# Optimization experiments

Measured on AMD Instinct MI355X. Metric: run time of the kernel, lower is better.

Reference implementation:

```python
import jax, jax.numpy as jnp
import numpy as np

D_MODEL = 1024
N_HEADS = 16
HEAD = D_MODEL // N_HEADS
B, T = 4, 2048


def setup_inputs() -> dict:
    key = jax.random.key(0)
    ks = jax.random.split(key, 8)
    s = 0.02
    return {
        "x_enc": jax.random.normal(ks[0], (B, T, D_MODEL), dtype=jnp.float32),
        "x_dec": jax.random.normal(ks[1], (B, T, D_MODEL), dtype=jnp.float32),
        "mask": jnp.zeros((B, T, T), dtype=jnp.float32),
        "Wq": jax.random.normal(ks[2], (D_MODEL, D_MODEL), dtype=jnp.float32) * s,
        "bq": jnp.zeros((D_MODEL,), dtype=jnp.float32),
        "Wkv": jax.random.normal(ks[3], (D_MODEL, 2 * D_MODEL), dtype=jnp.float32) * s,
        "bkv": jnp.zeros((2 * D_MODEL,), dtype=jnp.float32),
        "Wo": jax.random.normal(ks[4], (D_MODEL, D_MODEL), dtype=jnp.float32) * s,
        "bo": jnp.zeros((D_MODEL,), dtype=jnp.float32),
    }


def reference(x_enc, x_dec, mask, Wq, bq, Wkv, bkv, Wo, bo):
    b, t, c = x_enc.shape
    # projections
    kv = x_enc @ Wkv + bkv                     # [B,T,2C]
    q = x_dec @ Wq + bq                        # [B,T,C]
    # split heads (replicates torch reshape of interleaved kv)
    kv = kv.reshape(b, t, N_HEADS, 2 * HEAD).transpose(0, 2, 1, 3)  # [B,H,T,2hs]
    q = q.reshape(b, t, N_HEADS, HEAD).transpose(0, 2, 1, 3)        # [B,H,T,hs]
    k, v = kv[..., :HEAD], kv[..., HEAD:]
    # attention
    scores = jnp.einsum("bhqd,bhkd->bhqk", q, k) / np.sqrt(HEAD).astype(np.float32)
    scores = scores + mask[:, None, :, :]      # additive mask, broadcast over heads
    attn = jax.nn.softmax(scores, axis=-1)
    res = jnp.einsum("bhqk,bhkd->bhqd", attn, v)   # [B,H,T,hs]
    res = res.transpose(0, 2, 1, 3).reshape(b, t, c)
    return res @ Wo + bo
```

## Files before the change

kernel.cpp:

```cpp
#include <hip/hip_runtime.h>
#include <hip/hip_bf16.h>
#include <math.h>


#define D_MODEL 1024
#define NH      16
#define HEAD    64
#define BATCH   4
#define SEQ     2048
#define QB      256

#define LOG2E   1.44269504088896f

typedef unsigned int   u32;
typedef unsigned short u16;
typedef __attribute__((ext_vector_type(8))) short s16x8;
typedef __attribute__((ext_vector_type(4))) float f32x4;
typedef __attribute__((ext_vector_type(4))) unsigned int u32v4;

__device__ __forceinline__ u16 tobf(float f) {
    u32 u = __builtin_bit_cast(u32, f);
    return (u16)((u + 0x7fffu + ((u >> 16) & 1u)) >> 16);
}
__device__ __forceinline__ float frombf(u16 u) {
    return __builtin_bit_cast(float, (u32)u << 16);
}
__device__ __forceinline__ u32 cvtpk(float a, float b) {
    u32 r;
    asm("v_cvt_pk_bf16_f32 %0, %1, %2" : "=v"(r) : "v"(a), "v"(b));
    return r;
}
__device__ __forceinline__ float fexp2(float x) {
    float r;
    asm("v_exp_f32 %0, %1" : "=v"(r) : "v"(x));
    return r;
}

__device__ __forceinline__ void gl_lds16(const void* g, void* l) {
    __builtin_amdgcn_global_load_lds(
        (const __attribute__((address_space(1))) u32*)g,
        (__attribute__((address_space(3))) u32*)l, 16, 0, 0);
}

__global__ __launch_bounds__(256) void prep_all(
    const float* __restrict__ x_enc, const float* __restrict__ x_dec,
    u16* __restrict__ xout, int n,
    const float* __restrict__ Wq,  u16* __restrict__ wqT,
    const float* __restrict__ Wkv, u16* __restrict__ wkvT,
    const float* __restrict__ Wo,  u16* __restrict__ woT)
{
    __shared__ __align__(16) float tile[32][33];
    const int bid = blockIdx.x;
    if (bid < 16384) {
        const int y  = bid >> 13;
        const int bx = bid & 8191;
        const float* in = y ? x_dec : x_enc;
        u16* o = xout + (size_t)y * n;
        int i = (bx * 256 + threadIdx.x) * 4;
        if (i < n) {
            float4 v = *(const float4*)(in + i);
            ushort4 ov = make_ushort4(tobf(v.x), tobf(v.y), tobf(v.z), tobf(v.w));
            *(ushort4*)(o + i) = ov;
        }
        return;
    }
    const int tb = bid - 16384;
    const int z  = tb >> 10;
    const int rb = tb & 1023;
    const int bxT = rb & 31, byT = rb >> 5;
    const int K = D_MODEL;
    const float* W = (z == 0) ? Wq : (z == 3) ? Wo : Wkv;
    u16* WT       = (z == 0) ? wqT : (z == 3) ? woT : wkvT;
    const int N   = (z == 1 || z == 2) ? 2*D_MODEL : D_MODEL;
    const int nb  = (z == 2) ? D_MODEL : 0;
    const int n0 = nb + bxT * 32, k0 = byT * 32;
    const int r = threadIdx.x >> 3, c4 = (threadIdx.x & 7) * 4;
    float4 v = *(const float4*)&W[(size_t)(k0 + r) * N + n0 + c4];
    tile[r][c4] = v.x; tile[r][c4+1] = v.y; tile[r][c4+2] = v.z; tile[r][c4+3] = v.w;
    __syncthreads();
    ushort4 o = make_ushort4(tobf(tile[c4+0][r]), tobf(tile[c4+1][r]),
                             tobf(tile[c4+2][r]), tobf(tile[c4+3][r]));
    *(ushort4*)&WT[(size_t)(n0 + r) * K + k0 + c4] = o;
}

__global__ __launch_bounds__(256) void mask_prep(
    const float* __restrict__ mask, u16* __restrict__ mp)
{
    const size_t gt = (size_t)blockIdx.x * 256 + threadIdx.x;
    const int l = (int)(gt & 63);
    const size_t tile = gt >> 6;
    const int kt = (int)(tile & 127);
    const size_t bq = tile >> 7;
    const int qt = (int)(bq & 127);
    const int b  = (int)(bq >> 7);
    const int q15 = l & 15, quad = l >> 4;
    const int q = qt*16 + q15;
    const int k = (kt >> 2)*64 + ((kt >> 1) & 1)*32 + (kt & 1)*4 + quad*8;
    float4 v = *(const float4*)&mask[((size_t)(b*SEQ + q))*SEQ + k];
    ushort4 o = make_ushort4(tobf(v.x * LOG2E), tobf(v.y * LOG2E),
                             tobf(v.z * LOG2E), tobf(v.w * LOG2E));
    *(ushort4*)&mp[tile*256 + (size_t)l*4] = o;
}

__device__ __forceinline__ void xcd_swz(int& bx, int& by) {
    const int gx = gridDim.x;
    const int nwg = gx * gridDim.y;
    const int orig = by * gx + bx;
    const int swz = (orig & 7) * (nwg >> 3) + (orig >> 3);
    bx = swz % gx; by = swz / gx;
}

__device__ __forceinline__ void store_out(u16* p, float v)  { *p = tobf(v); }
__device__ __forceinline__ void store_out(float* p, float v){ *p = v; }

template <typename OT>
__global__ __launch_bounds__(256) void gemm_bt(
    const u16* __restrict__ A, const u16* __restrict__ Bt,
    const float* __restrict__ bias, OT* __restrict__ C,
    int N, int K, float out_scale)
{
    __shared__ __align__(16) u16 As[2][128 * 32];
    __shared__ __align__(16) u16 Bs[2][128 * 32];
    const int t = threadIdx.x;
    const int w = t >> 6, l = t & 63;
    const int lane15 = l & 15, quad = l >> 4;
    int bx = blockIdx.x, by = blockIdx.y;
    xcd_swz(bx, by);
    const int m0 = by * 128, n0 = bx * 128;
    const int wm = (w >> 1) * 64, wn = (w & 1) * 64;
    const int lr = l >> 2, lk = (l & 3) * 8;

    auto stage = [&](int k0, int bufi) {
        #pragma unroll
        for (int i = 0; i < 2; ++i) {
            const int chunk = w * 2 + i;
            gl_lds16(A  + (size_t)(m0 + chunk*16 + lr) * K + k0 + lk,
                     &As[bufi][chunk * 512]);
            gl_lds16(Bt + (size_t)(n0 + chunk*16 + lr) * K + k0 + lk,
                     &Bs[bufi][chunk * 512]);
        }
    };

    f32x4 acc[4][4] = {};
    const int nb = K >> 5;
    stage(0, 0);

    for (int i = 0; i < nb; ++i) {
        const int cur = i & 1;
        __syncthreads();
        if (i + 1 < nb) stage((i + 1) << 5, cur ^ 1);
        s16x8 af[4], bfr[4];
        #pragma unroll
        for (int i2 = 0; i2 < 4; ++i2)
            af[i2] = *(const s16x8*)&As[cur][(wm + i2*16 + lane15) * 32 + quad * 8];
        #pragma unroll
        for (int j = 0; j < 4; ++j)
            bfr[j] = *(const s16x8*)&Bs[cur][(wn + j*16 + lane15) * 32 + quad * 8];
        #pragma unroll
        for (int i2 = 0; i2 < 4; ++i2)
            #pragma unroll
            for (int j = 0; j < 4; ++j)
                acc[i2][j] = __builtin_amdgcn_mfma_f32_16x16x32_bf16(
                    af[i2], bfr[j], acc[i2][j], 0, 0, 0);
    }
    #pragma unroll
    for (int j = 0; j < 4; ++j) {
        const int col = n0 + wn + j*16 + lane15;
        const float bv = bias[col];
        #pragma unroll
        for (int i = 0; i < 4; ++i)
            #pragma unroll
            for (int r = 0; r < 4; ++r) {
                const int row = m0 + wm + i*16 + quad*4 + r;
                store_out(C + (size_t)row * N + col, (acc[i][j][r] + bv) * out_scale);
            }
    }
}

__global__ __launch_bounds__(512, 1) void gemm_kvq256(
    const u16* __restrict__ xe, const u16* __restrict__ xd,
    const u16* __restrict__ wkvT, const u16* __restrict__ wqT,
    const float* __restrict__ bkv, const float* __restrict__ bq,
    u16* __restrict__ kvb, u16* __restrict__ vtb, u16* __restrict__ qbuf)
{
    const int K = D_MODEL;
    const int NT = K / 64;
    __shared__ __align__(16) u16 sm[65536];
    u16* const smA = sm;
    u16* const smB = sm + 32768;
    const int t = threadIdx.x;
    const int w = t >> 6, l = t & 63;
    const int lane15 = l & 15, quad = l >> 4;
    int bx = blockIdx.x, by = blockIdx.y;
    xcd_swz(bx, by);
    const bool isq = bx >= 8;
    const u16* A  = isq ? xd : xe;
    const u16* Bt = isq ? wqT : wkvT;
    const int n0 = (isq ? bx - 8 : bx) * 256;
    const int m0 = by * 256;
    const int wm = (w >> 2) * 128;
    const int wn = (w & 3) * 64;
    const int lr = l >> 2;
    const int lc8 = (((l & 3) ^ (lr & 3)) * 8);
    const int cq  = (quad ^ (lane15 & 3)) * 8;

    auto stageA = [&](int tt, int s) {
        const int base = ((tt & 1) * 2 + s) * 256;
        const int k0 = tt * 64 + s * 32;
        #pragma unroll
        for (int jj = 0; jj < 2; ++jj) {
            const int r0 = jj * 128 + w * 16;
            gl_lds16(A + (size_t)(m0 + r0 + lr) * K + k0 + lc8,
                     smA + (base + r0) * 32);
        }
    };
    auto stageB = [&](int tt, int s) {
        const int base = ((tt & 1) * 2 + s) * 256;
        const int k0 = tt * 64 + s * 32;
        #pragma unroll
        for (int jj = 0; jj < 2; ++jj) {
            const int r0 = jj * 128 + w * 16;
            gl_lds16(Bt + (size_t)(n0 + r0 + lr) * K + k0 + lc8,
                     smB + (base + r0) * 32);
        }
    };

    f32x4 acc[8][4] = {};

    stageB(0,0); stageA(0,0); stageB(0,1); stageA(0,1);
    stageB(1,0); stageA(1,0); stageB(1,1);
    asm volatile("s_waitcnt vmcnt(6)" ::: "memory");
    __builtin_amdgcn_sched_barrier(0);
    __builtin_amdgcn_s_barrier();

    for (int tt = 0; tt < NT; ++tt) {
        const int p = tt & 1;
        const u16* Ab = smA + p * 16384;
        const u16* Bb = smB + p * 16384;
        s16x8 af[4], bfr[4];
        #pragma unroll
        for (int ph = 0; ph < 4; ++ph) {
            const int s = ph >> 1;
            const int ih = (ph & 1) * 4;
            #pragma unroll
            for (int i = 0; i < 4; ++i)
                af[i] = *(const s16x8*)(Ab + s*8192 + (wm + (ih + i)*16 + lane15)*32 + cq);
            if ((ph & 1) == 0) {
                #pragma unroll
                for (int j = 0; j < 4; ++j)
                    bfr[j] = *(const s16x8*)(Bb + s*8192 + (wn + j*16 + lane15)*32 + cq);
            }
            if (ph == 0)      { if (tt + 1 < NT) stageA(tt + 1, 1); }
            else if (ph == 1) { if (tt + 2 < NT) stageB(tt + 2, 0); }
            else if (ph == 2) { if (tt + 2 < NT) stageA(tt + 2, 0); }
            else              { if (tt + 2 < NT) stageB(tt + 2, 1); }
            __builtin_amdgcn_sched_barrier(0);
            __builtin_amdgcn_s_barrier();
            asm volatile("s_waitcnt lgkmcnt(0)" ::: "memory");
            __builtin_amdgcn_sched_barrier(0);
            __builtin_amdgcn_s_setprio(1);
            #pragma unroll
            for (int i = 0; i < 4; ++i)
                #pragma unroll
                for (int j = 0; j < 4; ++j)
                    acc[ih + i][j] = __builtin_amdgcn_mfma_f32_16x16x32_bf16(
                        af[i], bfr[j], acc[ih + i][j], 0, 0, 0);
            __builtin_amdgcn_s_setprio(0);
            __builtin_amdgcn_sched_barrier(0);
            if (ph == 3 && tt + 1 < NT) {
                if (tt + 2 < NT) asm volatile("s_waitcnt vmcnt(6)" ::: "memory");
                else             asm volatile("s_waitcnt vmcnt(0)" ::: "memory");
                __builtin_amdgcn_sched_barrier(0);
            }
            __builtin_amdgcn_s_barrier();
        }
    }

    if (isq) {
        const float sc = 0.125f * LOG2E;
        #pragma unroll
        for (int j = 0; j < 4; ++j) {
            const int col = n0 + wn + j*16 + lane15;
            const float bv = bq[col];
            #pragma unroll
            for (int i = 0; i < 8; ++i)
                #pragma unroll
                for (int r = 0; r < 4; ++r) {
                    const int row = m0 + wm + i*16 + quad*4 + r;
                    qbuf[(size_t)row * D_MODEL + col] = tobf((acc[i][j][r] + bv) * sc);
                }
        }
    } else if ((wn & 64) == 0) {
        #pragma unroll
        for (int j = 0; j < 4; ++j) {
            const int col = n0 + wn + j*16 + lane15;
            const float bv = bkv[col];
            #pragma unroll
            for (int i = 0; i < 8; ++i)
                #pragma unroll
                for (int r = 0; r < 4; ++r) {
                    const int row = m0 + wm + i*16 + quad*4 + r;
                    kvb[(size_t)row * (2*D_MODEL) + col] = tobf(acc[i][j][r] + bv);
                }
        }
    } else {
        const int head = (n0 + wn) >> 7;
        const int bh = (m0 >> 11) * NH + head;
        #pragma unroll
        for (int j = 0; j < 4; ++j) {
            const int d = j*16 + lane15;
            const float bv = bkv[n0 + wn + j*16 + lane15];
            #pragma unroll
            for (int i = 0; i < 8; ++i) {
                const int row = m0 + wm + i*16 + quad*4;
                const int tk = row & (SEQ - 1);
                u16* pp = vtb + ((size_t)bh*64 + d)*SEQ + tk;
                *(uint2*)pp = make_uint2(cvtpk(acc[i][j][0]+bv, acc[i][j][1]+bv),
                                         cvtpk(acc[i][j][2]+bv, acc[i][j][3]+bv));
            }
        }
    }
}

__global__ __launch_bounds__(512, 4) void attn_mfma(
    const u16* __restrict__ qb, const u16* __restrict__ kvb,
    const u16* __restrict__ vt, const u16* __restrict__ mp,
    u16* __restrict__ resb)
{
    __shared__ __align__(16) u16 sm[4*4096];
    const int t = threadIdx.x;
    const int w = t >> 6, l = t & 63;
    const int lane15 = l & 15, quad = l >> 4;
    const int h  = blockIdx.x;
    const int q0 = blockIdx.y * QB;
    const int b  = blockIdx.z;
    const int bh = b * NH + h;
    const int lr4 = l >> 2;
    const int lc8 = (((l & 3) ^ (lr4 & 3)) * 8);
    const int cq  = (quad ^ (lane15 & 3)) * 8;
    const int kprow = (lr4 >> 2)*8 + (lr4 & 3);

    s16x8 aq0[2], aq1[2];
    #pragma unroll
    for (int s = 0; s < 2; ++s) {
        const u16* qrow = qb + (size_t)(b*SEQ + q0 + w*32 + s*16 + lane15) * D_MODEL + h*HEAD;
        aq0[s] = *(const s16x8*)(qrow + quad*8);
        aq1[s] = *(const s16x8*)(qrow + 32 + quad*8);
    }
    const u16* mrow[2];
    #pragma unroll
    for (int s = 0; s < 2; ++s)
        mrow[s] = mp + (((size_t)b*128 + (q0>>4) + w*2 + s) * 128) * 256 + (size_t)l*4;

    auto stage = [&](int k0s, int bf) {
        const int hh = w & 1, rr = w >> 1;
        const int krow = (rr >> 1)*32 + (rr & 1)*4 + kprow;
        const u16* kg = kvb + (size_t)(b*SEQ + k0s + krow) * (2*D_MODEL)
                            + h*128 + hh*32 + lc8;
        gl_lds16(kg, sm + bf*4096 + hh*2048 + rr*512);
        const u16* vg = vt + (size_t)(bh*64 + rr*16 + lr4) * SEQ
                           + k0s + hh*32 + lc8;
        gl_lds16(vg, sm + 8192 + bf*4096 + hh*2048 + rr*512);
    };

    f32x4 o_acc[2][4] = {};
    f32x4 l_acc[2] = {};
    ushort4 mreg[2][4];
    s16x8 vones;
    #pragma unroll
    for (int i = 0; i < 8; ++i) vones[i] = (short)0x3F80;

    stage(0, 0);
    #pragma unroll
    for (int s = 0; s < 2; ++s)
        #pragma unroll
        for (int nt = 0; nt < 4; ++nt)
            mreg[s][nt] = *(const ushort4*)(mrow[s] + (size_t)nt * 256);

    for (int it = 0; it < SEQ/64; ++it) {
        const int k0 = it * 64;
        const int bf = it & 1;
        __syncthreads();
        if (it + 1 < SEQ/64)
            stage(k0 + 64, bf ^ 1);

        f32x4 sv[2][4];
        #pragma unroll
        for (int s = 0; s < 2; ++s)
            #pragma unroll
            for (int nt = 0; nt < 4; ++nt) {
                sv[s][nt][0] = frombf(mreg[s][nt].x); sv[s][nt][1] = frombf(mreg[s][nt].y);
                sv[s][nt][2] = frombf(mreg[s][nt].z); sv[s][nt][3] = frombf(mreg[s][nt].w);
            }
        __builtin_amdgcn_s_setprio(1);
        #pragma unroll
        for (int nt = 0; nt < 4; ++nt) {
            s16x8 kf0 = *(const s16x8*)(sm + bf*4096 +        (nt*16 + lane15)*32 + cq);
            s16x8 kf1 = *(const s16x8*)(sm + bf*4096 + 2048 + (nt*16 + lane15)*32 + cq);
            #pragma unroll
            for (int s = 0; s < 2; ++s) {
                sv[s][nt] = __builtin_amdgcn_mfma_f32_16x16x32_bf16(kf0, aq0[s], sv[s][nt], 0, 0, 0);
                sv[s][nt] = __builtin_amdgcn_mfma_f32_16x16x32_bf16(kf1, aq1[s], sv[s][nt], 0, 0, 0);
            }
        }
        __builtin_amdgcn_s_setprio(0);

        if (it + 1 < SEQ/64) {
            #pragma unroll
            for (int s = 0; s < 2; ++s)
                #pragma unroll
                for (int nt = 0; nt < 4; ++nt)
                    mreg[s][nt] = *(const ushort4*)(mrow[s] + ((size_t)((k0+64)>>4) + nt) * 256);
        }

        s16x8 pf[2][2];
        #pragma unroll
        for (int s = 0; s < 2; ++s)
            #pragma unroll
            for (int hf = 0; hf < 2; ++hf) {
                u32v4 pk;
                pk[0] = cvtpk(fexp2(sv[s][2*hf][0]),   fexp2(sv[s][2*hf][1]));
                pk[1] = cvtpk(fexp2(sv[s][2*hf][2]),   fexp2(sv[s][2*hf][3]));
                pk[2] = cvtpk(fexp2(sv[s][2*hf+1][0]), fexp2(sv[s][2*hf+1][1]));
                pk[3] = cvtpk(fexp2(sv[s][2*hf+1][2]), fexp2(sv[s][2*hf+1][3]));
                pf[s][hf] = __builtin_bit_cast(s16x8, pk);
            }

        __builtin_amdgcn_s_setprio(1);
        #pragma unroll
        for (int s = 0; s < 2; ++s) {
            l_acc[s] = __builtin_amdgcn_mfma_f32_16x16x32_bf16(vones, pf[s][0], l_acc[s], 0, 0, 0);
            l_acc[s] = __builtin_amdgcn_mfma_f32_16x16x32_bf16(vones, pf[s][1], l_acc[s], 0, 0, 0);
        }
        #pragma unroll
        for (int dt = 0; dt < 4; ++dt) {
            s16x8 vf0 = *(const s16x8*)(sm + 8192 + bf*4096 +        (dt*16 + lane15)*32 + cq);
            s16x8 vf1 = *(const s16x8*)(sm + 8192 + bf*4096 + 2048 + (dt*16 + lane15)*32 + cq);
            #pragma unroll
            for (int s = 0; s < 2; ++s) {
                o_acc[s][dt] = __builtin_amdgcn_mfma_f32_16x16x32_bf16(vf0, pf[s][0], o_acc[s][dt], 0, 0, 0);
                o_acc[s][dt] = __builtin_amdgcn_mfma_f32_16x16x32_bf16(vf1, pf[s][1], o_acc[s][dt], 0, 0, 0);
            }
        }
        __builtin_amdgcn_s_setprio(0);
    }

    __syncthreads();
    #pragma unroll
    for (int s = 0; s < 2; ++s) {
        const float inv = 1.f / l_acc[s][0];
        u16* orow = &sm[(w*32 + s*16 + lane15) * 64];
        #pragma unroll
        for (int dt = 0; dt < 4; ++dt) {
            *(uint2*)&orow[dt*16 + quad*4] = make_uint2(
                cvtpk(o_acc[s][dt][0]*inv, o_acc[s][dt][1]*inv),
                cvtpk(o_acc[s][dt][2]*inv, o_acc[s][dt][3]*inv));
        }
    }
    __syncthreads();
    {
        const int tr = t >> 1, tc = (t & 1) * 32;
        u16* o = resb + (size_t)(b*SEQ + q0 + tr) * D_MODEL + h*HEAD + tc;
        #pragma unroll
        for (int j = 0; j < 4; ++j)
            *(uint4*)(o + j*8) = *(const uint4*)&sm[tr*64 + tc + j*8];
    }
}

extern "C" void kernel_launch(void* const* d_in, const int* in_sizes, int n_in,
                              void* d_out, int out_size, void* d_ws, size_t ws_size,
                              hipStream_t stream) {
    const float* x_enc = (const float*)d_in[0];
    const float* x_dec = (const float*)d_in[1];
    const float* mask  = (const float*)d_in[2];
    const float* Wq    = (const float*)d_in[3];
    const float* bq    = (const float*)d_in[4];
    const float* Wkv   = (const float*)d_in[5];
    const float* bkv   = (const float*)d_in[6];
    const float* Wo    = (const float*)d_in[7];
    const float* bo    = (const float*)d_in[8];
    float* out = (float*)d_out;

    const int M = BATCH * SEQ;
    u16* xe   = (u16*)d_ws;
    u16* xd   = xe   + (size_t)M * D_MODEL;
    u16* wqT  = xd   + (size_t)M * D_MODEL;
    u16* wkvT = wqT  + (size_t)D_MODEL * D_MODEL;
    u16* woT  = wkvT + (size_t)2*D_MODEL*D_MODEL;
    u16* qbuf = woT  + (size_t)D_MODEL * D_MODEL;
    u16* kvb  = qbuf + (size_t)M * D_MODEL;
    u16* vtb  = kvb  + (size_t)M * 2 * D_MODEL;
    u16* resb = vtb  + (size_t)BATCH*NH*HEAD*SEQ;
    u16* mpk  = xe;

    const int NX = M * D_MODEL;
    prep_all<<<16384 + 4096, 256, 0, stream>>>(
        x_enc, x_dec, xe, NX, Wq, wqT, Wkv, wkvT, Wo, woT);

    gemm_kvq256<<<dim3(12, 32), 512, 0, stream>>>(
        xe, xd, wkvT, wqT, bkv, bq, kvb, vtb, qbuf);
    mask_prep<<<(BATCH*128*128*64)/256, 256, 0, stream>>>(mask, mpk);
    attn_mfma<<<dim3(NH, SEQ/QB, BATCH), 512, 0, stream>>>(
        qbuf, kvb, vtb, mpk, resb);
    gemm_bt<float><<<dim3(D_MODEL/128, M/128), 256, 0, stream>>>(
        resb, woT, bo, out, D_MODEL, D_MODEL, 1.0f);
}
```

Measured before the change: 366.8 us.

## Halve attention query tile and stage mask conversion through shared memory

The attention kernel's query tile per block drops from 256 to 128 rows, so each wave handles one 16-row query slice instead of two. This doubles the grid and cuts registers per wave, at the cost of loading each K/V tile twice as often per query. The mask_prep kernel now reads contiguous 16x512 mask rows with coalesced float4 loads into LDS, then writes the swizzled bf16 layout, replacing the previous scattered per-thread reads.

```diff
diff --git a/kernel.cpp b/kernel.cpp
--- a/kernel.cpp
+++ b/kernel.cpp
@@ -8,7 +8,7 @@
 #define HEAD    64
 #define BATCH   4
 #define SEQ     2048
-#define QB      256
+#define QB      128
 
 #define LOG2E   1.44269504088896f
 
@@ -86,20 +86,29 @@
 __global__ __launch_bounds__(256) void mask_prep(
     const float* __restrict__ mask, u16* __restrict__ mp)
 {
-    const size_t gt = (size_t)blockIdx.x * 256 + threadIdx.x;
-    const int l = (int)(gt & 63);
-    const size_t tile = gt >> 6;
-    const int kt = (int)(tile & 127);
-    const size_t bq = tile >> 7;
-    const int qt = (int)(bq & 127);
-    const int b  = (int)(bq >> 7);
+    __shared__ __align__(16) u16 ms[16][520];
+    const int t = threadIdx.x;
+    const int w = t >> 6, l = t & 63;
+    const int qt = blockIdx.x, kseg = blockIdx.y, b = blockIdx.z;
+    const float* src = mask + ((size_t)(b*SEQ + qt*16))*SEQ + kseg*512;
+    #pragma unroll
+    for (int p = 0; p < 8; ++p) {
+        const int idx = p*256 + t;
+        const int row = idx >> 7, c4 = (idx & 127) * 4;
+        float4 v = *(const float4*)(src + (size_t)row*SEQ + c4);
+        ushort4 o = make_ushort4(tobf(v.x*LOG2E), tobf(v.y*LOG2E),
+                                 tobf(v.z*LOG2E), tobf(v.w*LOG2E));
+        *(ushort4*)&ms[row][c4] = o;
+    }
+    __syncthreads();
     const int q15 = l & 15, quad = l >> 4;
-    const int q = qt*16 + q15;
-    const int k = (kt >> 2)*64 + ((kt >> 1) & 1)*32 + (kt & 1)*4 + quad*8;
-    float4 v = *(const float4*)&mask[((size_t)(b*SEQ + q))*SEQ + k];
-    ushort4 o = make_ushort4(tobf(v.x * LOG2E), tobf(v.y * LOG2E),
-                             tobf(v.z * LOG2E), tobf(v.w * LOG2E));
-    *(ushort4*)&mp[tile*256 + (size_t)l*4] = o;
+    u16* dst = mp + (((size_t)b*128 + qt)*128 + (size_t)kseg*32)*256 + (size_t)l*4;
+    #pragma unroll
+    for (int i = 0; i < 8; ++i) {
+        const int ktp = w*8 + i;
+        const int klocal = (ktp>>2)*64 + ((ktp>>1)&1)*32 + (ktp&1)*4 + quad*8;
+        *(uint2*)(dst + (size_t)ktp*256) = *(const uint2*)&ms[q15][klocal];
+    }
 }
 
 __device__ __forceinline__ void xcd_swz(int& bx, int& by) {
@@ -340,17 +349,10 @@
     const int cq  = (quad ^ (lane15 & 3)) * 8;
     const int kprow = (lr4 >> 2)*8 + (lr4 & 3);
 
-    s16x8 aq0[2], aq1[2];
-    #pragma unroll
-    for (int s = 0; s < 2; ++s) {
-        const u16* qrow = qb + (size_t)(b*SEQ + q0 + w*32 + s*16 + lane15) * D_MODEL + h*HEAD;
-        aq0[s] = *(const s16x8*)(qrow + quad*8);
-        aq1[s] = *(const s16x8*)(qrow + 32 + quad*8);
-    }
-    const u16* mrow[2];
-    #pragma unroll
-    for (int s = 0; s < 2; ++s)
-        mrow[s] = mp + (((size_t)b*128 + (q0>>4) + w*2 + s) * 128) * 256 + (size_t)l*4;
+    const u16* qrow = qb + (size_t)(b*SEQ + q0 + w*16 + lane15) * D_MODEL + h*HEAD;
+    s16x8 aq0 = *(const s16x8*)(qrow + quad*8);
+    s16x8 aq1 = *(const s16x8*)(qrow + 32 + quad*8);
+    const u16* mrow = mp + (((size_t)b*128 + (q0>>4) + w) * 128) * 256 + (size_t)l*4;
 
     auto stage = [&](int k0s, int bf) {
         const int hh = w & 1, rr = w >> 1;
@@ -363,19 +365,17 @@
         gl_lds16(vg, sm + 8192 + bf*4096 + hh*2048 + rr*512);
     };
 
-    f32x4 o_acc[2][4] = {};
-    f32x4 l_acc[2] = {};
-    ushort4 mreg[2][4];
+    f32x4 o_acc[4] = {};
+    f32x4 l_acc = {};
+    ushort4 mreg[4];
     s16x8 vones;
     #pragma unroll
     for (int i = 0; i < 8; ++i) vones[i] = (short)0x3F80;
 
     stage(0, 0);
     #pragma unroll
-    for (int s = 0; s < 2; ++s)
-        #pragma unroll
-        for (int nt = 0; nt < 4; ++nt)
-            mreg[s][nt] = *(const ushort4*)(mrow[s] + (size_t)nt * 256);
+    for (int nt = 0; nt < 4; ++nt)
+        mreg[nt] = *(const ushort4*)(mrow + (size_t)nt * 256);
 
     for (int it = 0; it < SEQ/64; ++it) {
         const int k0 = it * 64;
@@ -384,86 +384,69 @@
         if (it + 1 < SEQ/64)
             stage(k0 + 64, bf ^ 1);
 
-        f32x4 sv[2][4];
-        #pragma unroll
-        for (int s = 0; s < 2; ++s)
-            #pragma unroll
-            for (int nt = 0; nt < 4; ++nt) {
-                sv[s][nt][0] = frombf(mreg[s][nt].x); sv[s][nt][1] = frombf(mreg[s][nt].y);
-                sv[s][nt][2] = frombf(mreg[s][nt].z); sv[s][nt][3] = frombf(mreg[s][nt].w);
-            }
+        f32x4 sv[4];
+        #pragma unroll
+        for (int nt = 0; nt < 4; ++nt) {
+            sv[nt][0] = frombf(mreg[nt].x); sv[nt][1] = frombf(mreg[nt].y);
+            sv[nt][2] = frombf(mreg[nt].z); sv[nt][3] = frombf(mreg[nt].w);
+        }
         __builtin_amdgcn_s_setprio(1);
         #pragma unroll
         for (int nt = 0; nt < 4; ++nt) {
             s16x8 kf0 = *(const s16x8*)(sm + bf*4096 +        (nt*16 + lane15)*32 + cq);
             s16x8 kf1 = *(const s16x8*)(sm + bf*4096 + 2048 + (nt*16 + lane15)*32 + cq);
-            #pragma unroll
-            for (int s = 0; s < 2; ++s) {
-                sv[s][nt] = __builtin_amdgcn_mfma_f32_16x16x32_bf16(kf0, aq0[s], sv[s][nt], 0, 0, 0);
-                sv[s][nt] = __builtin_amdgcn_mfma_f32_16x16x32_bf16(kf1, aq1[s], sv[s][nt], 0, 0, 0);
-            }
+            sv[nt] = __builtin_amdgcn_mfma_f32_16x16x32_bf16(kf0, aq0, sv[nt], 0, 0, 0);
+            sv[nt] = __builtin_amdgcn_mfma_f32_16x16x32_bf16(kf1, aq1, sv[nt], 0, 0, 0);
         }
         __builtin_amdgcn_s_setprio(0);
 
         if (it + 1 < SEQ/64) {
             #pragma unroll
-            for (int s = 0; s < 2; ++s)
-                #pragma unroll
-                for (int nt = 0; nt < 4; ++nt)
-                    mreg[s][nt] = *(const ushort4*)(mrow[s] + ((size_t)((k0+64)>>4) + nt) * 256);
-        }
-
-        s16x8 pf[2][2];
-        #pragma unroll
-        for (int s = 0; s < 2; ++s)
-            #pragma unroll
-            for (int hf = 0; hf < 2; ++hf) {
-                u32v4 pk;
-                pk[0] = cvtpk(fexp2(sv[s][2*hf][0]),   fexp2(sv[s][2*hf][1]));
-                pk[1] = cvtpk(fexp2(sv[s][2*hf][2]),   fexp2(sv[s][2*hf][3]));
-                pk[2] = cvtpk(fexp2(sv[s][2*hf+1][0]), fexp2(sv[s][2*hf+1][1]));
-                pk[3] = cvtpk(fexp2(sv[s][2*hf+1][2]), fexp2(sv[s][2*hf+1][3]));
-                pf[s][hf] = __builtin_bit_cast(s16x8, pk);
-            }
+            for (int nt = 0; nt < 4; ++nt)
+                mreg[nt] = *(const ushort4*)(mrow + ((size_t)((k0+64)>>4) + nt) * 256);
+        }
+
+        s16x8 pf[2];
+        #pragma unroll
+        for (int hf = 0; hf < 2; ++hf) {
+            u32v4 pk;
+            pk[0] = cvtpk(fexp2(sv[2*hf][0]),   fexp2(sv[2*hf][1]));
+            pk[1] = cvtpk(fexp2(sv[2*hf][2]),   fexp2(sv[2*hf][3]));
+            pk[2] = cvtpk(fexp2(sv[2*hf+1][0]), fexp2(sv[2*hf+1][1]));
+            pk[3] = cvtpk(fexp2(sv[2*hf+1][2]), fexp2(sv[2*hf+1][3]));
+            pf[hf] = __builtin_bit_cast(s16x8, pk);
+        }
 
         __builtin_amdgcn_s_setprio(1);
-        #pragma unroll
-        for (int s = 0; s < 2; ++s) {
-            l_acc[s] = __builtin_amdgcn_mfma_f32_16x16x32_bf16(vones, pf[s][0], l_acc[s], 0, 0, 0);
-            l_acc[s] = __builtin_amdgcn_mfma_f32_16x16x32_bf16(vones, pf[s][1], l_acc[s], 0, 0, 0);
-        }
+        l_acc = __builtin_amdgcn_mfma_f32_16x16x32_bf16(vones, pf[0], l_acc, 0, 0, 0);
+        l_acc = __builtin_amdgcn_mfma_f32_16x16x32_bf16(vones, pf[1], l_acc, 0, 0, 0);
         #pragma unroll
         for (int dt = 0; dt < 4; ++dt) {
             s16x8 vf0 = *(const s16x8*)(sm + 8192 + bf*4096 +        (dt*16 + lane15)*32 + cq);
             s16x8 vf1 = *(const s16x8*)(sm + 8192 + bf*4096 + 2048 + (dt*16 + lane15)*32 + cq);
-            #pragma unroll
-            for (int s = 0; s < 2; ++s) {
-                o_acc[s][dt] = __builtin_amdgcn_mfma_f32_16x16x32_bf16(vf0, pf[s][0], o_acc[s][dt], 0, 0, 0);
-                o_acc[s][dt] = __builtin_amdgcn_mfma_f32_16x16x32_bf16(vf1, pf[s][1], o_acc[s][dt], 0, 0, 0);
-            }
+            o_acc[dt] = __builtin_amdgcn_mfma_f32_16x16x32_bf16(vf0, pf[0], o_acc[dt], 0, 0, 0);
+            o_acc[dt] = __builtin_amdgcn_mfma_f32_16x16x32_bf16(vf1, pf[1], o_acc[dt], 0, 0, 0);
         }
         __builtin_amdgcn_s_setprio(0);
     }
 
     __syncthreads();
-    #pragma unroll
-    for (int s = 0; s < 2; ++s) {
-        const float inv = 1.f / l_acc[s][0];
-        u16* orow = &sm[(w*32 + s*16 + lane15) * 64];
+    {
+        const float inv = 1.f / l_acc[0];
+        u16* orow = &sm[(w*16 + lane15) * 64];
         #pragma unroll
         for (int dt = 0; dt < 4; ++dt) {
             *(uint2*)&orow[dt*16 + quad*4] = make_uint2(
-                cvtpk(o_acc[s][dt][0]*inv, o_acc[s][dt][1]*inv),
-                cvtpk(o_acc[s][dt][2]*inv, o_acc[s][dt][3]*inv));
+                cvtpk(o_acc[dt][0]*inv, o_acc[dt][1]*inv),
+                cvtpk(o_acc[dt][2]*inv, o_acc[dt][3]*inv));
         }
     }
     __syncthreads();
     {
-        const int tr = t >> 1, tc = (t & 1) * 32;
+        const int tr = t >> 2, tc = (t & 3) * 16;
         u16* o = resb + (size_t)(b*SEQ + q0 + tr) * D_MODEL + h*HEAD + tc;
-        #pragma unroll
-        for (int j = 0; j < 4; ++j)
-            *(uint4*)(o + j*8) = *(const uint4*)&sm[tr*64 + tc + j*8];
+        *(uint4*)o       = *(const uint4*)&sm[tr*64 + tc];
+        *(uint4*)(o + 8) = *(const uint4*)&sm[tr*64 + tc + 8];
     }
 }
 
@@ -499,7 +482,7 @@
 
     gemm_kvq256<<<dim3(12, 32), 512, 0, stream>>>(
         xe, xd, wkvT, wqT, bkv, bq, kvb, vtb, qbuf);
-    mask_prep<<<(BATCH*128*128*64)/256, 256, 0, stream>>>(mask, mpk);
+    mask_prep<<<dim3(SEQ/16, 4, BATCH), 256, 0, stream>>>(mask, mpk);
     attn_mfma<<<dim3(NH, SEQ/QB, BATCH), 512, 0, stream>>>(
         qbuf, kvb, vtb, mpk, resb);
     gemm_bt<float><<<dim3(D_MODEL/128, M/128), 256, 0, stream>>>(
```

Result: slower. 378.0 us (+3.1%).
